# Performance work log

Measured on AMD Instinct MI355X. Metric: run time of the kernel, lower is better.

The kernel has to match this reference:

```python
import jax, jax.numpy as jnp
import numpy as np

B, T, C = 2, 2048, 2048
H, KVH, HD = 16, 4, 128  # heads, kv heads, head_dim
G = H // KVH             # GQA group size
THETA = 10000.0


def _rope_cos_sin(t, hd, dtype):
    inv_freq = 1.0 / (THETA ** (jnp.arange(0, hd, 2, dtype=jnp.float32) / hd))
    pos = jnp.arange(t, dtype=jnp.float32)
    freqs = pos[:, None] * inv_freq[None, :]          # [T, hd/2]
    emb = jnp.concatenate([freqs, freqs], axis=-1)    # [T, hd]
    return jnp.cos(emb).astype(dtype), jnp.sin(emb).astype(dtype)


def _rotate_half(x):
    x1, x2 = jnp.split(x, 2, axis=-1)
    return jnp.concatenate([-x2, x1], axis=-1)


def setup_inputs() -> dict:
    key = jax.random.key(0)
    ks = jax.random.split(key, 5)
    s_in = 1.0 / np.sqrt(C)
    return {
        "x": jax.random.normal(ks[0], (B, T, C), jnp.float32),
        "wq": jax.random.normal(ks[1], (C, H * HD), jnp.float32) * s_in,
        "bq": jnp.zeros((H * HD,), jnp.float32),
        "wk": jax.random.normal(ks[2], (C, KVH * HD), jnp.float32) * s_in,
        "bk": jnp.zeros((KVH * HD,), jnp.float32),
        "wv": jax.random.normal(ks[3], (C, KVH * HD), jnp.float32) * s_in,
        "bv": jnp.zeros((KVH * HD,), jnp.float32),
        "wo": jax.random.normal(ks[4], (H * HD, C), jnp.float32) * (1.0 / np.sqrt(H * HD)),
    }


def reference(x, wq, bq, wk, bk, wv, bv, wo):
    b, t, c = x.shape
    q = (x @ wq + bq).reshape(b, t, H, HD).transpose(0, 2, 1, 3)    # [B,H,T,hd]
    k = (x @ wk + bk).reshape(b, t, KVH, HD).transpose(0, 2, 1, 3)  # [B,KVH,T,hd]
    v = (x @ wv + bv).reshape(b, t, KVH, HD).transpose(0, 2, 1, 3)

    cos, sin = _rope_cos_sin(t, HD, x.dtype)  # [T,hd]
    q = q * cos + _rotate_half(q) * sin
    k = k * cos + _rotate_half(k) * sin

    # GQA: group query heads over kv heads
    qg = q.reshape(b, KVH, G, t, HD)
    scale = 1.0 / np.sqrt(HD)
    scores = jnp.einsum('bkgtd,bksd->bkgts', qg, k) * scale  # [B,KVH,G,T,T]
    causal = jnp.tril(jnp.ones((t, t), bool))
    scores = jnp.where(causal, scores, jnp.finfo(scores.dtype).min)
    attn = jax.nn.softmax(scores, axis=-1)
    out = jnp.einsum('bkgts,bksd->bkgtd', attn, v)            # [B,KVH,G,T,hd]
    out = out.reshape(b, H, t, HD).transpose(0, 2, 1, 3).reshape(b, t, H * HD)
    return out @ wo
```

## Files before the change

### kernel.cpp

```cpp
#include <hip/hip_runtime.h>
#include <hip/hip_bf16.h>
#include <math.h>

#define B_ 2
#define T_ 2048
#define C_ 2048
#define H_ 16
#define KVH_ 4
#define HD_ 128
#define G_ (H_ / KVH_)
#define MROWS (B_ * T_)
#define NQKV (H_ * HD_ + 2 * KVH_ * HD_)
#define KOFF (H_ * HD_)
#define VOFF (H_ * HD_ + KVH_ * HD_)
#define L2T (13.287712379549449f / 64.0f)

typedef __hip_bfloat16 bf16;
typedef short bf16x8 __attribute__((ext_vector_type(8)));
typedef short bf16x4 __attribute__((ext_vector_type(4)));
typedef float f32x4 __attribute__((ext_vector_type(4)));

__device__ __forceinline__ void gload_lds16(const void* g, void* l) {
  __builtin_amdgcn_global_load_lds(
      (const __attribute__((address_space(1))) unsigned int*)g,
      (__attribute__((address_space(3))) unsigned int*)l, 16, 0, 0);
}

static __device__ __forceinline__ f32x4 mfma32k(bf16x8 a, bf16x8 b, f32x4 c) {
  return __builtin_amdgcn_mfma_f32_16x16x32_bf16(a, b, c, 0, 0, 0);
}

static __device__ __forceinline__ short f2bf(float x) {
  unsigned u = __builtin_bit_cast(unsigned, x);
  u += 0x7FFFu + ((u >> 16) & 1u);
  return (short)(u >> 16);
}

static __device__ __forceinline__ float bfh2f(short h) {
  unsigned u = ((unsigned)(unsigned short)h) << 16;
  return __builtin_bit_cast(float, u);
}

static __device__ __forceinline__ float fexp2(float x) {
#if __has_builtin(__builtin_amdgcn_exp2f)
  return __builtin_amdgcn_exp2f(x);
#else
  return exp2f(x);
#endif
}

__global__ __launch_bounds__(256) void prep_kernel(
    const float* __restrict__ x, bf16* __restrict__ xb,
    const float* __restrict__ wq, const float* __restrict__ wk,
    const float* __restrict__ wv, bf16* __restrict__ wqkvT,
    const float* __restrict__ wo, bf16* __restrict__ woT,
    float2* __restrict__ tab) {
  __shared__ float t[32][33];
  int bid = blockIdx.x;
  if (bid < 8192) {
    const int i = (bid * 256 + threadIdx.x) * 4;
    float4 v = *(const float4*)(x + i);
    xb[i + 0] = __float2bfloat16(v.x);
    xb[i + 1] = __float2bfloat16(v.y);
    xb[i + 2] = __float2bfloat16(v.z);
    xb[i + 3] = __float2bfloat16(v.w);
    return;
  }
  bid -= 8192;
  if (bid < 6144) {
    const int tx = threadIdx.x & 31, ty = threadIdx.x >> 5;
    const int c0 = (bid % 96) * 32;
    const int r0 = (bid / 96) * 32;
    const float* src;
    int nn, ld;
    if (c0 < KOFF)      { src = wq; nn = c0;        ld = 2048; }
    else if (c0 < VOFF) { src = wk; nn = c0 - KOFF; ld = 512; }
    else                { src = wv; nn = c0 - VOFF; ld = 512; }
#pragma unroll
    for (int it = 0; it < 4; ++it)
      t[ty + 8 * it][tx] = src[(size_t)(r0 + ty + 8 * it) * ld + nn + tx];
    __syncthreads();
#pragma unroll
    for (int it = 0; it < 4; ++it)
      wqkvT[(size_t)(c0 + ty + 8 * it) * 2048 + r0 + tx] =
          __float2bfloat16(t[tx][ty + 8 * it]);
    return;
  }
  bid -= 6144;
  if (bid < 4096) {
    const int tx = threadIdx.x & 31, ty = threadIdx.x >> 5;
    const int c0 = (bid & 63) * 32;
    const int r0 = (bid >> 6) * 32;
#pragma unroll
    for (int it = 0; it < 4; ++it)
      t[ty + 8 * it][tx] = wo[(size_t)(r0 + ty + 8 * it) * 2048 + c0 + tx];
    __syncthreads();
#pragma unroll
    for (int it = 0; it < 4; ++it)
      woT[(size_t)(c0 + ty + 8 * it) * 2048 + r0 + tx] =
          __float2bfloat16(t[tx][ty + 8 * it]);
    return;
  }
  bid -= 4096;
  {
    const int idx = bid * 256 + threadIdx.x;
    const int tt = idx >> 6, i = idx & 63;
    const float invf = fexp2(-(float)i * L2T);
    float s, c;
    __sincosf((float)tt * invf, &s, &c);
    tab[idx] = make_float2(c, s);
  }
}

template <bool BF16OUT, bool FUSE>
__global__ __launch_bounds__(256, 2) void gemm_mfma64(
    const bf16* __restrict__ A, const bf16* __restrict__ Bt, void* __restrict__ Cout,
    const float* __restrict__ bq, const float* __restrict__ bk2,
    const float* __restrict__ bv2, int M, int N, int K,
    bf16* __restrict__ kp, bf16* __restrict__ vp, const float2* __restrict__ tab) {
  __shared__ __align__(16) short SH[2 * 128 * 64];
  short* As = SH;
  short* Bs = SH + 128 * 64;
  const int tid = threadIdx.x;
  const int w = tid >> 6, lane = tid & 63;
  const int colL = lane & 15, quad = lane >> 4;
  const int wm = w & 1, wn = w >> 1;
  const int r0 = blockIdx.y * 128, c0 = blockIdx.x * 128;
  const int lrow = lane >> 3;
  const int lsl = ((lane & 7) ^ lrow) * 8;
  const int c7 = colL & 7;
  const int sq0 = (quad ^ c7) * 8;
  const int sq1 = ((4 + quad) ^ c7) * 8;

  f32x4 acc[4][4];
  const f32x4 zero = {0.f, 0.f, 0.f, 0.f};
#pragma unroll
  for (int mt = 0; mt < 4; ++mt)
#pragma unroll
    for (int nt = 0; nt < 4; ++nt) acc[mt][nt] = zero;

  const bf16* pa = A + (size_t)(r0 + lrow) * K + lsl;
  const bf16* pb = Bt + (size_t)(c0 + lrow) * K + lsl;

  for (int k0 = 0; k0 < K; k0 += 64) {
    __syncthreads();
#pragma unroll
    for (int it = 0; it < 4; ++it) {
      const int seg = it * 4 + w;
      gload_lds16(pa + (size_t)seg * 8 * K + k0, &As[seg * 8 * 64]);
      gload_lds16(pb + (size_t)seg * 8 * K + k0, &Bs[seg * 8 * 64]);
    }
    __syncthreads();
#pragma unroll
    for (int ks = 0; ks < 2; ++ks) {
      const int sq = ks ? sq1 : sq0;
      bf16x8 af[4], bfv[4];
#pragma unroll
      for (int mt = 0; mt < 4; ++mt)
        af[mt] = *(const bf16x8*)&As[(wm * 64 + mt * 16 + colL) * 64 + sq];
#pragma unroll
      for (int nt = 0; nt < 4; ++nt)
        bfv[nt] = *(const bf16x8*)&Bs[(wn * 64 + nt * 16 + colL) * 64 + sq];
#pragma unroll
      for (int mt = 0; mt < 4; ++mt)
#pragma unroll
        for (int nt = 0; nt < 4; ++nt)
          acc[mt][nt] = mfma32k(af[mt], bfv[nt], acc[mt][nt]);
    }
  }

  if (!FUSE || c0 < KOFF) {
#pragma unroll
    for (int nt = 0; nt < 4; ++nt) {
      const int c = c0 + wn * 64 + nt * 16 + colL;
      float bias = 0.f;
      if (bq) bias = (c < KOFF) ? bq[c] : (c < VOFF ? bk2[c - KOFF] : bv2[c - VOFF]);
#pragma unroll
      for (int mt = 0; mt < 4; ++mt) {
#pragma unroll
        for (int i = 0; i < 4; ++i) {
          const int r = r0 + wm * 64 + mt * 16 + quad * 4 + i;
          const float v = acc[mt][nt][i] + bias;
          if (BF16OUT)
            ((bf16*)Cout)[(size_t)r * N + c] = __float2bfloat16(v);
          else
            ((float*)Cout)[(size_t)r * N + c] = v;
        }
      }
    }
  } else {
    __syncthreads();
    const bool isK = (c0 < VOFF);
#pragma unroll
    for (int nt = 0; nt < 4; ++nt) {
      const int c = c0 + wn * 64 + nt * 16 + colL;
      const float bias = isK ? bk2[c - KOFF] : bv2[c - VOFF];
      const int col = wn * 64 + nt * 16 + colL;
#pragma unroll
      for (int mt = 0; mt < 4; ++mt) {
#pragma unroll
        for (int i = 0; i < 4; ++i) {
          const int row = wm * 64 + mt * 16 + quad * 4 + i;
          SH[row * 128 + (col ^ ((row & 7) << 3))] = f2bf(acc[mt][nt][i] + bias);
        }
      }
    }
    __syncthreads();
    const int b = r0 >> 11;
    const int tbase = (r0 & 2047) >> 5;
    const int kvh = (c0 - (isK ? KOFF : VOFF)) >> 7;
    const int bkq = b * 4 + kvh;
    if (isK) {
#pragma unroll
      for (int s = 0; s < 8; ++s) {
        const int unit = s * 256 + tid;
        const int L = unit & 63, kc = (unit >> 6) & 7, tile = unit >> 9;
        const int trow = tile * 32 + ((L >> 2) & 3) * 8 + ((kc >> 2) << 2) + (L & 3);
        const int d = (kc & 3) * 32 + ((L >> 4) << 3);
        const int sx = (trow & 7) << 3;
        bf16x8 lo = *(const bf16x8*)&SH[trow * 128 + (d ^ sx)];
        bf16x8 hi = *(const bf16x8*)&SH[trow * 128 + ((d ^ 64) ^ sx)];
        const int t_abs = (r0 + trow) & (T_ - 1);
        const float2* tp = tab + t_abs * 64 + (d & 63);
        bf16x8 outv;
#pragma unroll
        for (int j = 0; j < 8; ++j) {
          const float2 cs = tp[j];
          const float a = bfh2f(lo[j]), p = bfh2f(hi[j]);
          outv[j] = f2bf((d < 64) ? (a * cs.x - p * cs.y) : (a * cs.x + p * cs.y));
        }
        *(bf16x8*)(kp + ((size_t)((bkq * 64 + tbase + tile) * 8 + kc)) * 512 + L * 8) = outv;
      }
    } else {
#pragma unroll
      for (int s = 0; s < 8; ++s) {
        const int unit = s * 256 + tid;
        const int L = unit & 63, ht = (unit >> 6) & 7, tile = unit >> 9;
        const int rowb = tile * 32 + ((L >> 4) << 3);
        const int colv = ht * 16 + (L & 15);
        bf16x8 v;
#pragma unroll
        for (int j = 0; j < 8; ++j)
          v[j] = SH[(rowb + j) * 128 + (colv ^ (((rowb + j) & 7) << 3))];
        *(bf16x8*)(vp + ((size_t)((bkq * 64 + tbase + tile) * 8 + ht)) * 512 + L * 8) = v;
      }
    }
  }
}

#define FA_SCL2 (0.08838834764831845f * 1.4426950408889634f)
#define FA_M2 16.0f

__global__ __launch_bounds__(256, 4) void flash_mfma8(
    const bf16* __restrict__ qkv, const bf16* __restrict__ kp,
    const bf16* __restrict__ vp, bf16* __restrict__ ao,
    const float2* __restrict__ tab) {
  __shared__ __align__(16) bf16 KS[3][4096];
  __shared__ __align__(16) bf16 VS[2][4096];

  const int id = blockIdx.x;
  const int bk = id & 7;
  const int u = id >> 3;
  const int jq = 127 - u;
  const int b = bk >> 2, kvh = bk & 3;
  const int w = threadIdx.x >> 6;
  const int h = (kvh << 2) | w;
  const int lane = threadIdx.x & 63;
  const int colL = lane & 15, quad = lane >> 4;
  const int myq0 = jq * 16;
  const int nkv = (jq >> 1) + 1;

  const bf16* kpt = kp + ((size_t)(bk * 64)) * 4096 + (w * 2) * 512 + lane * 8;
  const bf16* vpt = vp + ((size_t)(bk * 64)) * 4096 + (w * 2) * 512 + lane * 8;

  auto stageK = [&](int tile, int slot) {
    const bf16* s = kpt + (size_t)tile * 4096;
    bf16* d = &KS[slot][(w * 2) * 512];
    gload_lds16(s, d);
    gload_lds16(s + 512, d + 512);
  };
  auto stageV = [&](int tile, int slot) {
    const bf16* s = vpt + (size_t)tile * 4096;
    bf16* d = &VS[slot][(w * 2) * 512];
    gload_lds16(s, d);
    gload_lds16(s + 512, d + 512);
  };

  bf16x8 qf[4];
  {
    const bf16* qg = qkv + (size_t)(b * T_ + myq0) * NQKV + h * HD_;
    bf16x8 rq[4];
#pragma unroll
    for (int c = 0; c < 4; ++c)
      rq[c] = *(const bf16x8*)(qg + (size_t)colL * NQKV + c * 32 + quad * 8);
    const float2* tp = tab + (myq0 + colL) * 64 + quad * 8;
    float2 cs0[8], cs1[8];
#pragma unroll
    for (int jj = 0; jj < 8; ++jj) { cs0[jj] = tp[jj]; cs1[jj] = tp[32 + jj]; }
#pragma unroll
    for (int c = 0; c < 4; ++c) {
#pragma unroll
      for (int jj = 0; jj < 8; ++jj) {
        const float2 cs = (c & 1) ? cs1[jj] : cs0[jj];
        const float a = bfh2f(rq[c][jj]), p = bfh2f(rq[c ^ 2][jj]);
        qf[c][jj] = f2bf((c & 2) ? (a * cs.x + p * cs.y)
                                 : (a * cs.x - p * cs.y));
      }
    }
  }

  const f32x4 zero = {0.f, 0.f, 0.f, 0.f};
  auto qk = [&](const bf16* Kb, f32x4 (&s_)[2]) {
    s_[0] = zero; s_[1] = zero;
#pragma unroll
    for (int c = 0; c < 4; ++c) {
      bf16x8 kf0 = *(const bf16x8*)(Kb + c * 512 + lane * 8);
      bf16x8 kf1 = *(const bf16x8*)(Kb + (4 + c) * 512 + lane * 8);
      s_[0] = mfma32k(kf0, qf[c], s_[0]);
      s_[1] = mfma32k(kf1, qf[c], s_[1]);
    }
  };

  f32x4 o[8];
#pragma unroll
  for (int ht = 0; ht < 8; ++ht) o[ht] = zero;
  float l_ = 0.f;

  stageK(0, 0);
  if (nkv > 1) stageK(1, 1);
  if (nkv > 2) stageK(2, 2);
  stageV(0, 0);
  asm volatile("s_waitcnt vmcnt(0)\n\ts_barrier" ::: "memory");

  f32x4 sA[2], sB[2];
  qk(KS[0], sA);

  int kStage = 0, kNext = 1;
#pragma unroll 1
  for (int tt = 0; tt < nkv; ++tt) {
    const bool sv = (tt + 1 < nkv), sk = (tt + 3 < nkv);
    if (sv) stageV(tt + 1, (tt + 1) & 1);
    if (sk) stageK(tt + 3, kStage);

    if (sv) qk(KS[kNext], sB);

    bf16x4 pf[2];
    if (tt == nkv - 1) {
      const int qg = ((jq & 1) << 4) | colL;
#pragma unroll
      for (int kt = 0; kt < 2; ++kt) {
        const int kb = quad * 8 + kt * 4;
        float pv[4];
#pragma unroll
        for (int i = 0; i < 4; ++i) {
          float e = fexp2(fmaf(sA[kt][i], FA_SCL2, -FA_M2));
          pv[i] = (kb + i <= qg) ? e : 0.f;
        }
        l_ += (pv[0] + pv[1]) + (pv[2] + pv[3]);
        pf[kt] = (bf16x4){f2bf(pv[0]), f2bf(pv[1]), f2bf(pv[2]), f2bf(pv[3])};
      }
    } else {
#pragma unroll
      for (int kt = 0; kt < 2; ++kt) {
        float pv[4];
#pragma unroll
        for (int i = 0; i < 4; ++i)
          pv[i] = fexp2(fmaf(sA[kt][i], FA_SCL2, -FA_M2));
        l_ += (pv[0] + pv[1]) + (pv[2] + pv[3]);
        pf[kt] = (bf16x4){f2bf(pv[0]), f2bf(pv[1]), f2bf(pv[2]), f2bf(pv[3])};
      }
    }

    {
      const bf16* Vb = VS[tt & 1];
      const bf16x8 pcat = __builtin_shufflevector(pf[0], pf[1], 0, 1, 2, 3, 4, 5, 6, 7);
#pragma unroll
      for (int ht = 0; ht < 8; ++ht) {
        bf16x8 vf8 = *(const bf16x8*)(Vb + ht * 512 + lane * 8);
        o[ht] = mfma32k(vf8, pcat, o[ht]);
      }
    }

    if (sk) asm volatile("s_waitcnt vmcnt(2)\n\ts_barrier" ::: "memory");
    else    asm volatile("s_waitcnt vmcnt(0)\n\ts_barrier" ::: "memory");

    sA[0] = sB[0]; sA[1] = sB[1];
    kStage = (kStage == 2) ? 0 : kStage + 1;
    kNext  = (kNext == 2) ? 0 : kNext + 1;
  }

  {
    float lv = l_;
    lv += __shfl_xor(lv, 16);
    lv += __shfl_xor(lv, 32);
    const float rl = 1.f / lv;
    const size_t rbase = (size_t)(b * T_ + myq0 + colL) * (H_ * HD_) + h * HD_;
#pragma unroll
    for (int ht = 0; ht < 8; ++ht) {
      bf16x4 ov;
#pragma unroll
      for (int i = 0; i < 4; ++i) ov[i] = f2bf(o[ht][i] * rl);
      *(bf16x4*)(ao + rbase + ht * 16 + quad * 4) = ov;
    }
  }
}

extern "C" void kernel_launch(void* const* d_in, const int* in_sizes, int n_in,
                              void* d_out, int out_size, void* d_ws, size_t ws_size,
                              hipStream_t stream) {
  (void)in_sizes; (void)n_in; (void)out_size; (void)ws_size;
  const float* x  = (const float*)d_in[0];
  const float* wq = (const float*)d_in[1];
  const float* bq = (const float*)d_in[2];
  const float* wk = (const float*)d_in[3];
  const float* bk = (const float*)d_in[4];
  const float* wv = (const float*)d_in[5];
  const float* bv = (const float*)d_in[6];
  const float* wo = (const float*)d_in[7];
  float* out = (float*)d_out;

  char* ws = (char*)d_ws;
  bf16* xb    = (bf16*)ws;
  bf16* wqkvT = (bf16*)(ws + (16u << 20));
  bf16* woT   = (bf16*)(ws + (28u << 20));
  bf16* qkv   = (bf16*)(ws + (36u << 20));
  bf16* kp    = (bf16*)(ws + (60u << 20));
  bf16* vp    = (bf16*)(ws + (68u << 20));
  float2* tab = (float2*)(ws + (76u << 20));

  prep_kernel<<<dim3(18944), dim3(256), 0, stream>>>(
      x, xb, wq, wk, wv, wqkvT, wo, woT, tab);

  gemm_mfma64<true, true><<<dim3(NQKV / 128, MROWS / 128), dim3(256), 0, stream>>>(
      xb, wqkvT, qkv, bq, bk, bv, MROWS, NQKV, C_, kp, vp, tab);

  bf16* ao = xb;
  flash_mfma8<<<dim3(1024), dim3(256), 0, stream>>>(qkv, kp, vp, ao, tab);

  gemm_mfma64<false, false><<<dim3(C_ / 128, MROWS / 128), dim3(256), 0, stream>>>(
      ao, woT, out, nullptr, nullptr, nullptr, MROWS, C_, KOFF,
      nullptr, nullptr, nullptr);
}
```

Baseline: 287.0 us.

## Load V tiles straight into registers and drop the V LDS buffers

```diff
diff --git a/kernel.cpp b/kernel.cpp
--- a/kernel.cpp
+++ b/kernel.cpp
@@ -251,12 +251,11 @@
 #define FA_SCL2 (0.08838834764831845f * 1.4426950408889634f)
 #define FA_M2 16.0f
 
-__global__ __launch_bounds__(256, 4) void flash_mfma8(
+__global__ __launch_bounds__(256, 5) void flash_mfma8(
     const bf16* __restrict__ qkv, const bf16* __restrict__ kp,
     const bf16* __restrict__ vp, bf16* __restrict__ ao,
     const float2* __restrict__ tab) {
   __shared__ __align__(16) bf16 KS[3][4096];
-  __shared__ __align__(16) bf16 VS[2][4096];
 
   const int id = blockIdx.x;
   const int bk = id & 7;
@@ -271,7 +270,7 @@
   const int nkv = (jq >> 1) + 1;
 
   const bf16* kpt = kp + ((size_t)(bk * 64)) * 4096 + (w * 2) * 512 + lane * 8;
-  const bf16* vpt = vp + ((size_t)(bk * 64)) * 4096 + (w * 2) * 512 + lane * 8;
+  const bf16* vbase = vp + ((size_t)(bk * 64)) * 4096 + lane * 8;
 
   auto stageK = [&](int tile, int slot) {
     const bf16* s = kpt + (size_t)tile * 4096;
@@ -279,12 +278,6 @@
     gload_lds16(s, d);
     gload_lds16(s + 512, d + 512);
   };
-  auto stageV = [&](int tile, int slot) {
-    const bf16* s = vpt + (size_t)tile * 4096;
-    bf16* d = &VS[slot][(w * 2) * 512];
-    gload_lds16(s, d);
-    gload_lds16(s + 512, d + 512);
-  };
 
   bf16x8 qf[4];
   {
@@ -329,7 +322,6 @@
   stageK(0, 0);
   if (nkv > 1) stageK(1, 1);
   if (nkv > 2) stageK(2, 2);
-  stageV(0, 0);
   asm volatile("s_waitcnt vmcnt(0)\n\ts_barrier" ::: "memory");
 
   f32x4 sA[2], sB[2];
@@ -338,11 +330,18 @@
   int kStage = 0, kNext = 1;
 #pragma unroll 1
   for (int tt = 0; tt < nkv; ++tt) {
-    const bool sv = (tt + 1 < nkv), sk = (tt + 3 < nkv);
-    if (sv) stageV(tt + 1, (tt + 1) & 1);
+    const bool sk = (tt + 3 < nkv);
+
+    bf16x8 vr[8];
+    {
+      const bf16* vsrc = vbase + (size_t)tt * 4096;
+#pragma unroll
+      for (int ht = 0; ht < 8; ++ht)
+        vr[ht] = *(const bf16x8*)(vsrc + ht * 512);
+    }
     if (sk) stageK(tt + 3, kStage);
 
-    if (sv) qk(KS[kNext], sB);
+    if (tt + 1 < nkv) qk(KS[kNext], sB);
 
     bf16x4 pf[2];
     if (tt == nkv - 1) {
@@ -372,17 +371,13 @@
     }
 
     {
-      const bf16* Vb = VS[tt & 1];
       const bf16x8 pcat = __builtin_shufflevector(pf[0], pf[1], 0, 1, 2, 3, 4, 5, 6, 7);
 #pragma unroll
-      for (int ht = 0; ht < 8; ++ht) {
-        bf16x8 vf8 = *(const bf16x8*)(Vb + ht * 512 + lane * 8);
-        o[ht] = mfma32k(vf8, pcat, o[ht]);
-      }
-    }
-
-    if (sk) asm volatile("s_waitcnt vmcnt(2)\n\ts_barrier" ::: "memory");
-    else    asm volatile("s_waitcnt vmcnt(0)\n\ts_barrier" ::: "memory");
+      for (int ht = 0; ht < 8; ++ht)
+        o[ht] = mfma32k(vr[ht], pcat, o[ht]);
+    }
+
+    __builtin_amdgcn_s_barrier();
 
     sA[0] = sB[0]; sA[1] = sB[1];
     kStage = (kStage == 2) ? 0 : kStage + 1;
```

Result: slower. 305.3 us (+6.4%).
